# Performance work log

Hardware: AMD Instinct MI355X
Metric: run time of the kernel (lower is better)

## Reference

```python
import jax, jax.numpy as jnp
import numpy as np

BS, N, D = 8, 2048, 512


def setup_inputs() -> dict:
    key = jax.random.key(0)
    ks = jax.random.split(key, 8)
    s = 0.05  # small scale keeps exp(k + bias) numerically tame
    inp = jax.random.normal(ks[0], (BS, N, D), dtype=jnp.float32)
    Wq = jax.random.normal(ks[1], (D, D), dtype=jnp.float32) * s
    bq = jax.random.normal(ks[2], (D,), dtype=jnp.float32) * s
    Wk = jax.random.normal(ks[3], (D, D), dtype=jnp.float32) * s
    bk = jax.random.normal(ks[4], (D,), dtype=jnp.float32) * s
    Wv = jax.random.normal(ks[5], (D, D), dtype=jnp.float32) * s
    bv = jax.random.normal(ks[6], (D,), dtype=jnp.float32) * s
    pos_bias = jax.random.normal(ks[7], (N, N), dtype=jnp.float32) * s
    return {"input": inp, "Wq": Wq, "bq": bq, "Wk": Wk, "bk": bk,
            "Wv": Wv, "bv": bv, "pos_bias": pos_bias}


def reference(input, Wq, bq, Wk, bk, Wv, bv, pos_bias):
    # q, k, v projections: (bs, n, d)
    q = input @ Wq + bq
    k = input @ Wk + bk
    v = input @ Wv + bv
    # AFT-Full: out[b,i,d] = sigmoid(q)[b,i,d] *
    #   sum_j exp(k[b,j,d] + B[i,j]) * v[b,j,d] / sum_j exp(k[b,j,d] + B[i,j])
    # Factor exp(k + B) = exp(B) * exp(k): avoids the (n,bs,n,d) broadcast,
    # identical math to the torch source.
    ek = jnp.exp(k)                       # (bs, n, d)
    eB = jnp.exp(pos_bias)                # (n, n), rows = query pos i
    numerator = jnp.einsum('ij,bjd->bid', eB, ek * v)
    denominator = jnp.einsum('ij,bjd->bid', eB, ek)
    return jax.nn.sigmoid(q) * (numerator / denominator)
```

## Files before the change

### kernel.cpp

```cpp
#include <hip/hip_runtime.h>
#include <stdint.h>

#define N_SEQ 2048
#define D_MODEL 512
#define MROWS 16384
#define NT_K 32

typedef __attribute__((ext_vector_type(8))) short bf16x8;
typedef __attribute__((ext_vector_type(4))) float f32x4;
typedef __attribute__((ext_vector_type(16))) float f32x16;

__device__ __forceinline__ short f2bf(float f) {
  union { float f; uint32_t u; } x; x.f = f;
  uint32_t r = x.u + 0x7FFFu + ((x.u >> 16) & 1u);
  return (short)(uint16_t)(r >> 16);
}
__device__ __forceinline__ unsigned short f2h(float f) {
  union { _Float16 h; unsigned short u; } x; x.h = (_Float16)f; return x.u;
}
__device__ __forceinline__ float h2f(unsigned short u) {
  union { unsigned short u; _Float16 h; } x; x.u = u; return (float)x.h;
}

__device__ __forceinline__ void gload_lds16(const void* g, void* l) {
  __builtin_amdgcn_global_load_lds(
      (__attribute__((address_space(1))) void*)(void*)g,
      (__attribute__((address_space(3))) void*)l, 16, 0, 0);
}


__global__ void k_conv_bf16(const float* __restrict__ in,
                            short* __restrict__ a, int n4) {
  int stride = gridDim.x * blockDim.x;
  for (int i = blockIdx.x * blockDim.x + threadIdx.x; i < n4; i += stride) {
    float4 v = reinterpret_cast<const float4*>(in)[i];
    short4 h;
    h.x = f2bf(v.x); h.y = f2bf(v.y); h.z = f2bf(v.z); h.w = f2bf(v.w);
    reinterpret_cast<short4*>(a)[i] = h;
  }
}

__global__ void k_prep_eb(const float* __restrict__ pb, short* __restrict__ eb,
                          int n4) {
  int stride = gridDim.x * blockDim.x;
  for (int i = blockIdx.x * blockDim.x + threadIdx.x; i < n4; i += stride) {
    float4 v = reinterpret_cast<const float4*>(pb)[i];
    short4 o;
    o.x = f2bf(expf(v.x));
    o.y = f2bf(expf(v.y));
    o.z = f2bf(expf(v.z));
    o.w = f2bf(expf(v.w));
    reinterpret_cast<short4*>(eb)[i] = o;
  }
}

__global__ void k_prep_w(const float* __restrict__ Wq, const float* __restrict__ Wk,
                         const float* __restrict__ Wv, short* __restrict__ wh) {
  int t = blockIdx.x * blockDim.x + threadIdx.x;
  if (t >= 1536 * 512) return;
  int c = t >> 9, k = t & 511;
  float v;
  if (c < 512) v = Wq[k * 512 + c];
  else {
    int cc = c - 512, d = cc >> 1;
    v = (cc & 1) ? Wv[k * 512 + d] : Wk[k * 512 + d];
  }
  wh[t] = f2bf(v);
}

__global__ __launch_bounds__(256) void k_proj(
    const short* __restrict__ A, const short* __restrict__ W,
    const float* __restrict__ bq, const float* __restrict__ bk,
    const float* __restrict__ bv,
    unsigned short* __restrict__ sigq, short* __restrict__ Xf) {
  __shared__ short lA[128 * 64], lB[128 * 64];
  const int tid = threadIdx.x;
  const int lane = tid & 63, wid = tid >> 6;
  const int wr = wid >> 1, wc = wid & 1;
  const int lrow = lane & 15;
  const int kq = (lane >> 4) << 4;
  const int row0 = blockIdx.x * 128;
  const int col0 = blockIdx.y * 128;

  const f32x4 fzero = {0.f, 0.f, 0.f, 0.f};
  f32x4 acc[4][4];
#pragma unroll
  for (int m = 0; m < 4; ++m)
#pragma unroll
    for (int n = 0; n < 4; ++n) acc[m][n] = fzero;

  const short* gA = A + row0 * 512;
  const short* gB = W + col0 * 512;

  for (int kt = 0; kt < 8; ++kt) {
    const int kb = kt * 64;
#pragma unroll
    for (int p = 0; p < 4; ++p) {
      int c = p * 256 + tid;
      int B = c << 4;
      int r = B >> 7;
      int wp = (B & 127) ^ ((r & 7) << 4);
      int ke = wp >> 1;
      int goff = r * 512 + kb + ke;
      int loff = (p * 256 + wid * 64) << 3;
      gload_lds16(gA + goff, lA + loff);
      gload_lds16(gB + goff, lB + loff);
    }
    __syncthreads();
#pragma unroll
    for (int ks = 0; ks < 2; ++ks) {
      int kb2 = kq + ks * 64;
      bf16x8 fb[4];
#pragma unroll
      for (int n = 0; n < 4; ++n) {
        int r = wc * 64 + n * 16 + lrow;
        fb[n] = *(const bf16x8*)((const char*)lB + (r << 7) +
                                 (kb2 ^ ((r & 7) << 4)));
      }
#pragma unroll
      for (int m = 0; m < 4; ++m) {
        int r = wr * 64 + m * 16 + lrow;
        bf16x8 fa = *(const bf16x8*)((const char*)lA + (r << 7) +
                                     (kb2 ^ ((r & 7) << 4)));
#pragma unroll
        for (int n = 0; n < 4; ++n)
          acc[m][n] = __builtin_amdgcn_mfma_f32_16x16x32_bf16(fa, fb[n], acc[m][n], 0, 0, 0);
      }
    }
    __syncthreads();
  }

  const int rbase = row0 + wr * 64 + ((lane >> 4) << 2);
  if (col0 < 512) {
#pragma unroll
    for (int n = 0; n < 4; ++n) {
      int c = col0 + wc * 64 + n * 16 + lrow;
      float bias = bq[c];
#pragma unroll
      for (int m = 0; m < 4; ++m) {
        int gr = rbase + m * 16;
#pragma unroll
        for (int r = 0; r < 4; ++r) {
          float q = acc[m][n][r] + bias;
          sigq[(gr + r) * 512 + c] = f2h(1.f / (1.f + expf(-q)));
        }
      }
    }
  } else {
    int s = lane & 1;
#pragma unroll
    for (int n = 0; n < 4; ++n) {
      int c = col0 + wc * 64 + n * 16 + lrow;
      int d = (c - 512) >> 1;
      float bias = s ? bv[d] : bk[d];
#pragma unroll
      for (int m = 0; m < 4; ++m) {
        int gr = rbase + m * 16;
        int b = gr >> 11;
        int j = gr & 2047;
        f32x4 val;
#pragma unroll
        for (int r = 0; r < 4; ++r) val[r] = acc[m][n][r] + bias;
        if (!s) {
#pragma unroll
          for (int r = 0; r < 4; ++r) val[r] = expf(val[r]);
        }
        f32x4 oth;
#pragma unroll
        for (int r = 0; r < 4; ++r) oth[r] = __shfl_xor(val[r], 1);
        if (!s) {
          short4 wq, eq;
          wq.x = f2bf(val[0] * oth[0]); eq.x = f2bf(val[0]);
          wq.y = f2bf(val[1] * oth[1]); eq.y = f2bf(val[1]);
          wq.z = f2bf(val[2] * oth[2]); eq.z = f2bf(val[2]);
          wq.w = f2bf(val[3] * oth[3]); eq.w = f2bf(val[3]);
          int colp = b * 1024 + 2 * d;
          int kg16 = j >> 4;
          int lnn = (colp & 31) + (((j >> 3) & 1) << 5);
          int e0 = j & 7;
          size_t base = ((size_t)kg16 << 17) + (((size_t)(colp >> 5)) << 9);
          *(short4*)&Xf[base + (lnn << 3) + e0] = wq;
          *(short4*)&Xf[base + ((lnn + 1) << 3) + e0] = eq;
        }
      }
    }
  }
}

__global__ __launch_bounds__(512, 4) void k_main8(
    const short* __restrict__ eB, const short* __restrict__ Xf,
    const unsigned short* __restrict__ sigq, float* __restrict__ out) {
  extern __shared__ short lds[];
  const int tid = threadIdx.x;
  const int lane = tid & 63, wid = tid >> 6;
  const int wr = wid >> 1, wc = wid & 1;
  const int l31 = lane & 31;
  const int lhi = lane >> 5;

  const int bid = blockIdx.x;
  const int xcd = bid & 7, bj = bid >> 3;
  const int row0 = (bj & 7) * 256;
  const int col0 = ((xcd << 3) + (bj >> 3)) * 128;

  f32x16 acc[2][2];
#pragma unroll
  for (int m = 0; m < 2; ++m)
#pragma unroll
    for (int n = 0; n < 2; ++n)
#pragma unroll
      for (int r = 0; r < 16; ++r) acc[m][n][r] = 0.f;

  const short* gA = eB + row0 * 2048;
  const int pfo = ((col0 >> 5) + wc * 2) * 512 + (lane << 3);

  auto STAGE = [&](int kt) {
    const short* src = gA + kt * 64;
    const int sb = (kt & 1) << 14;
#pragma unroll
    for (int p = 0; p < 4; ++p) {
      int c = p * 512 + tid;
      int r = c >> 3;
      int ke = ((((c & 7) << 4) ^ (((c >> 3) & 7) << 4)) >> 1);
      gload_lds16(src + r * 2048 + ke,
                  lds + sb + ((p * 512 + wid * 64) << 3));
    }
  };
  auto LDA = [&](int b, int ks, int m) -> bf16x8 {
    int R = wr * 64 + m * 32 + l31;
    int kb = ks * 32 + (lhi << 4);
    return *(const bf16x8*)((const char*)lds + (b << 15) + R * 128 +
                            (kb ^ ((R & 7) << 4)));
  };
  auto LOADFB = [&](bf16x8* fb, int kt, int h) {
#pragma unroll
    for (int k2 = 0; k2 < 2; ++k2) {
      const short* base = Xf + (((size_t)(kt * 4 + h * 2 + k2)) << 17) + pfo;
      fb[k2 * 2 + 0] = *(const bf16x8*)(base);
      fb[k2 * 2 + 1] = *(const bf16x8*)(base + 512);
    }
  };

  bf16x8 fb[8];

  STAGE(0);
  LOADFB(fb, 0, 0);
  LOADFB(fb + 4, 0, 1);
  __syncthreads();

  for (int t = 0; t < NT_K; ++t) {
    const int b = t & 1;
    if (t + 1 < NT_K) STAGE(t + 1);
    {
      bf16x8 fa[4];
#pragma unroll
      for (int k2 = 0; k2 < 2; ++k2)
#pragma unroll
        for (int m = 0; m < 2; ++m) fa[k2 * 2 + m] = LDA(b, k2, m);
      __builtin_amdgcn_s_setprio(1);
#pragma unroll
      for (int k2 = 0; k2 < 2; ++k2)
#pragma unroll
        for (int m = 0; m < 2; ++m)
#pragma unroll
          for (int n = 0; n < 2; ++n)
            acc[m][n] = __builtin_amdgcn_mfma_f32_32x32x16_bf16(
                fa[k2 * 2 + m], fb[k2 * 2 + n], acc[m][n], 0, 0, 0);
      __builtin_amdgcn_s_setprio(0);
    }
    if (t + 1 < NT_K) LOADFB(fb, t + 1, 0);
    {
      bf16x8 fa[4];
#pragma unroll
      for (int k2 = 0; k2 < 2; ++k2)
#pragma unroll
        for (int m = 0; m < 2; ++m) fa[k2 * 2 + m] = LDA(b, 2 + k2, m);
      __builtin_amdgcn_s_setprio(1);
#pragma unroll
      for (int k2 = 0; k2 < 2; ++k2)
#pragma unroll
        for (int m = 0; m < 2; ++m)
#pragma unroll
          for (int n = 0; n < 2; ++n)
            acc[m][n] = __builtin_amdgcn_mfma_f32_32x32x16_bf16(
                fa[k2 * 2 + m], fb[4 + k2 * 2 + n], acc[m][n], 0, 0, 0);
      __builtin_amdgcn_s_setprio(0);
    }
    if (t + 1 < NT_K) LOADFB(fb + 4, t + 1, 1);
    __syncthreads();
  }

  const int rb32 = row0 + wr * 64 + (lhi << 2);
#pragma unroll
  for (int n = 0; n < 2; ++n) {
    int c = col0 + wc * 64 + n * 32 + l31;
    int b = c >> 10;
    int d = (c & 1023) >> 1;
#pragma unroll
    for (int m = 0; m < 2; ++m) {
      f32x16 den;
#pragma unroll
      for (int r = 0; r < 16; ++r) den[r] = __shfl_xor(acc[m][n][r], 1);
      if ((lane & 1) == 0) {
#pragma unroll
        for (int r = 0; r < 16; ++r) {
          int i2 = rb32 + m * 32 + (r & 3) + ((r >> 2) << 3);
          int idx = (b * 2048 + i2) * 512 + d;
          out[idx] = h2f(sigq[idx]) * (acc[m][n][r] / den[r]);
        }
      }
    }
  }
}

extern "C" void kernel_launch(void* const* d_in, const int* in_sizes, int n_in,
                              void* d_out, int out_size, void* d_ws, size_t ws_size,
                              hipStream_t stream) {
  const float* in = (const float*)d_in[0];
  const float* Wq = (const float*)d_in[1];
  const float* bq = (const float*)d_in[2];
  const float* Wk = (const float*)d_in[3];
  const float* bk = (const float*)d_in[4];
  const float* Wv = (const float*)d_in[5];
  const float* bv = (const float*)d_in[6];
  const float* pb = (const float*)d_in[7];
  float* out = (float*)d_out;

  char* ws = (char*)d_ws;
  short* Xf = (short*)ws;
  short* eB = (short*)(ws + 33554432);
  short* Ah = (short*)(ws + 41943040);
  short* Wh = (short*)(ws + 58720256);
  unsigned short* sigq = (unsigned short*)(ws + 60293120);

  (void)hipFuncSetAttribute((const void*)k_main8,
                            hipFuncAttributeMaxDynamicSharedMemorySize, 65536);

  k_conv_bf16<<<2048, 256, 0, stream>>>(in, Ah, MROWS * D_MODEL / 4);
  k_prep_w<<<3072, 256, 0, stream>>>(Wq, Wk, Wv, Wh);
  k_prep_eb<<<2048, 256, 0, stream>>>(pb, eB, N_SEQ * N_SEQ / 4);

  dim3 gp(128, 12);
  k_proj<<<gp, 256, 0, stream>>>(Ah, Wh, bq, bk, bv, sigq, Xf);

  k_main8<<<dim3(512), 512, 65536, stream>>>(eB, Xf, sigq, out);
}
```

Measured before the change: 165.8 us.

## Pre-swizzle exp(pos_bias) into MFMA fragment layout and drop LDS staging

The exp(pos_bias) prep kernel now writes the bf16 result directly in a fragment-major layout that matches the MFMA A-operand. The main GEMM kernel then loads A fragments straight from global memory, as it already does for B, instead of staging tiles through LDS with async global-to-LDS copies and barriers. This removes all shared memory use and __syncthreads from the main loop, which may raise occupancy and cut sync overhead. In exchange, A fragments are read from global or L2 by each wave with no LDS reuse across the two column waves, and the A loads are issued just before their MFMAs with no prefetch, so latency may be exposed.

```diff
diff --git a/kernel.cpp b/kernel.cpp
--- a/kernel.cpp
+++ b/kernel.cpp
@@ -40,17 +40,23 @@
   }
 }
 
-__global__ void k_prep_eb(const float* __restrict__ pb, short* __restrict__ eb,
-                          int n4) {
+__global__ void k_prep_ebf(const float* __restrict__ pb,
+                           short* __restrict__ ebf) {
   int stride = gridDim.x * blockDim.x;
-  for (int i = blockIdx.x * blockDim.x + threadIdx.x; i < n4; i += stride) {
-    float4 v = reinterpret_cast<const float4*>(pb)[i];
+  for (int t = blockIdx.x * blockDim.x + threadIdx.x; t < N_SEQ * N_SEQ / 4;
+       t += stride) {
+    int i = t >> 9;
+    int j = (t & 511) << 2;
+    float4 v = reinterpret_cast<const float4*>(pb)[t];
     short4 o;
     o.x = f2bf(expf(v.x));
     o.y = f2bf(expf(v.y));
     o.z = f2bf(expf(v.z));
     o.w = f2bf(expf(v.w));
-    reinterpret_cast<short4*>(eb)[i] = o;
+    int kg16 = j >> 4;
+    int ln = (i & 31) + (((j >> 3) & 1) << 5);
+    int e0 = j & 7;
+    *(short4*)&ebf[(kg16 << 15) + ((i >> 5) << 9) + (ln << 3) + e0] = o;
   }
 }
 
@@ -187,10 +193,9 @@
   }
 }
 
-__global__ __launch_bounds__(512, 4) void k_main8(
-    const short* __restrict__ eB, const short* __restrict__ Xf,
+__global__ __launch_bounds__(512, 4) void k_main9(
+    const short* __restrict__ eBf, const short* __restrict__ Xf,
     const unsigned short* __restrict__ sigq, float* __restrict__ out) {
-  extern __shared__ short lds[];
   const int tid = threadIdx.x;
   const int lane = tid & 63, wid = tid >> 6;
   const int wr = wid >> 1, wc = wid & 1;
@@ -210,52 +215,34 @@
 #pragma unroll
       for (int r = 0; r < 16; ++r) acc[m][n][r] = 0.f;
 
-  const short* gA = eB + row0 * 2048;
-  const int pfo = ((col0 >> 5) + wc * 2) * 512 + (lane << 3);
-
-  auto STAGE = [&](int kt) {
-    const short* src = gA + kt * 64;
-    const int sb = (kt & 1) << 14;
-#pragma unroll
-    for (int p = 0; p < 4; ++p) {
-      int c = p * 512 + tid;
-      int r = c >> 3;
-      int ke = ((((c & 7) << 4) ^ (((c >> 3) & 7) << 4)) >> 1);
-      gload_lds16(src + r * 2048 + ke,
-                  lds + sb + ((p * 512 + wid * 64) << 3));
-    }
-  };
-  auto LDA = [&](int b, int ks, int m) -> bf16x8 {
-    int R = wr * 64 + m * 32 + l31;
-    int kb = ks * 32 + (lhi << 4);
-    return *(const bf16x8*)((const char*)lds + (b << 15) + R * 128 +
-                            (kb ^ ((R & 7) << 4)));
+  const int pfa = ((row0 >> 5) + wr * 2) * 512 + (lane << 3);
+  const int pfb = ((col0 >> 5) + wc * 2) * 512 + (lane << 3);
+
+  auto LOADFA = [&](bf16x8* fa, int kt, int h) {
+#pragma unroll
+    for (int k2 = 0; k2 < 2; ++k2) {
+      const short* base = eBf + (((size_t)(kt * 4 + h * 2 + k2)) << 15) + pfa;
+      fa[k2 * 2 + 0] = *(const bf16x8*)(base);
+      fa[k2 * 2 + 1] = *(const bf16x8*)(base + 512);
+    }
   };
   auto LOADFB = [&](bf16x8* fb, int kt, int h) {
 #pragma unroll
     for (int k2 = 0; k2 < 2; ++k2) {
-      const short* base = Xf + (((size_t)(kt * 4 + h * 2 + k2)) << 17) + pfo;
+      const short* base = Xf + (((size_t)(kt * 4 + h * 2 + k2)) << 17) + pfb;
       fb[k2 * 2 + 0] = *(const bf16x8*)(base);
       fb[k2 * 2 + 1] = *(const bf16x8*)(base + 512);
     }
   };
 
   bf16x8 fb[8];
-
-  STAGE(0);
   LOADFB(fb, 0, 0);
   LOADFB(fb + 4, 0, 1);
-  __syncthreads();
 
   for (int t = 0; t < NT_K; ++t) {
-    const int b = t & 1;
-    if (t + 1 < NT_K) STAGE(t + 1);
     {
       bf16x8 fa[4];
-#pragma unroll
-      for (int k2 = 0; k2 < 2; ++k2)
-#pragma unroll
-        for (int m = 0; m < 2; ++m) fa[k2 * 2 + m] = LDA(b, k2, m);
+      LOADFA(fa, t, 0);
       __builtin_amdgcn_s_setprio(1);
 #pragma unroll
       for (int k2 = 0; k2 < 2; ++k2)
@@ -270,10 +257,7 @@
     if (t + 1 < NT_K) LOADFB(fb, t + 1, 0);
     {
       bf16x8 fa[4];
-#pragma unroll
-      for (int k2 = 0; k2 < 2; ++k2)
-#pragma unroll
-        for (int m = 0; m < 2; ++m) fa[k2 * 2 + m] = LDA(b, 2 + k2, m);
+      LOADFA(fa, t, 1);
       __builtin_amdgcn_s_setprio(1);
 #pragma unroll
       for (int k2 = 0; k2 < 2; ++k2)
@@ -286,7 +270,6 @@
       __builtin_amdgcn_s_setprio(0);
     }
     if (t + 1 < NT_K) LOADFB(fb + 4, t + 1, 1);
-    __syncthreads();
   }
 
   const int rb32 = row0 + wr * 64 + (lhi << 2);
@@ -327,20 +310,17 @@
 
   char* ws = (char*)d_ws;
   short* Xf = (short*)ws;
-  short* eB = (short*)(ws + 33554432);
+  short* eBf = (short*)(ws + 33554432);
   short* Ah = (short*)(ws + 41943040);
   short* Wh = (short*)(ws + 58720256);
   unsigned short* sigq = (unsigned short*)(ws + 60293120);
 
-  (void)hipFuncSetAttribute((const void*)k_main8,
-                            hipFuncAttributeMaxDynamicSharedMemorySize, 65536);
-
   k_conv_bf16<<<2048, 256, 0, stream>>>(in, Ah, MROWS * D_MODEL / 4);
   k_prep_w<<<3072, 256, 0, stream>>>(Wq, Wk, Wv, Wh);
-  k_prep_eb<<<2048, 256, 0, stream>>>(pb, eB, N_SEQ * N_SEQ / 4);
+  k_prep_ebf<<<2048, 256, 0, stream>>>(pb, eBf);
 
   dim3 gp(128, 12);
   k_proj<<<gp, 256, 0, stream>>>(Ah, Wh, bq, bk, bv, sigq, Xf);
 
-  k_main8<<<dim3(512), 512, 65536, stream>>>(eB, Xf, sigq, out);
-}
+  k_main9<<<dim3(512), 512, 0, stream>>>(eBf, Xf, sigq, out);
+}
```

Result: slower. 176.6 us (+6.6%).
